# Optimization experiments

Measured on AMD Instinct MI355X. Metric: run time of the kernel, lower is better.

The kernel has to match this reference:

```python
import jax, jax.numpy as jnp
import numpy as np

B, N, NR, D = 1024, 100000, 500, 200
OC, FW = 32, 9          # out_channels, filt_w (filt_h is always 1)
L = D - FW + 1          # 192, conv output width
EPS = 1e-5


def setup_inputs() -> dict:
    key = jax.random.key(0)
    ks = jax.random.split(key, 22)
    inp = {
        "e1_idx": jax.random.randint(ks[0], (B,), 0, N),
        "r_idx": jax.random.randint(ks[1], (B,), 0, NR),
        "E": jax.random.normal(ks[2], (N, D), jnp.float32) * 0.1,
        "R": jax.random.normal(ks[3], (NR, D), jnp.float32) * 0.1,
        "W_fc": jax.random.normal(ks[4], (OC * L, D), jnp.float32) * 0.02,
        "b_fc": jnp.zeros((D,), jnp.float32),
        "W_fc1": jax.random.normal(ks[5], (D, OC * FW), jnp.float32) * 0.05,
        "b_fc1": jnp.zeros((OC * FW,), jnp.float32),
        "bn0_g": jax.random.uniform(ks[6], (1,), jnp.float32, 0.5, 1.5),
        "bn0_b": jax.random.normal(ks[7], (1,), jnp.float32) * 0.1,
        "bn0_m": jax.random.normal(ks[8], (1,), jnp.float32) * 0.1,
        "bn0_v": jax.random.uniform(ks[9], (1,), jnp.float32, 0.5, 1.5),
        "bn1_g": jax.random.uniform(ks[10], (OC,), jnp.float32, 0.5, 1.5),
        "bn1_b": jax.random.normal(ks[11], (OC,), jnp.float32) * 0.1,
        "bn1_m": jax.random.normal(ks[12], (OC,), jnp.float32) * 0.1,
        "bn1_v": jax.random.uniform(ks[13], (OC,), jnp.float32, 0.5, 1.5),
        "bn2_g": jax.random.uniform(ks[14], (D,), jnp.float32, 0.5, 1.5),
        "bn2_b": jax.random.normal(ks[15], (D,), jnp.float32) * 0.1,
        "bn2_m": jax.random.normal(ks[16], (D,), jnp.float32) * 0.1,
        "bn2_v": jax.random.uniform(ks[17], (D,), jnp.float32, 0.5, 1.5),
        "b": jnp.zeros((N,), jnp.float32),
    }
    return inp


def reference(e1_idx, r_idx, E, R, W_fc, b_fc, W_fc1, b_fc1,
              bn0_g, bn0_b, bn0_m, bn0_v,
              bn1_g, bn1_b, bn1_m, bn1_v,
              bn2_g, bn2_b, bn2_m, bn2_v, b):
    # embeddings
    e1 = E[e1_idx]                       # [B, D]  (the [B,1,1,D] image)
    r = R[r_idx]                         # [B, D]
    # bn0 over the single input channel (eval mode, running stats)
    x = (e1 - bn0_m) * (bn0_g / jnp.sqrt(bn0_v + EPS)) + bn0_b   # [B, D]
    # hypernetwork: per-sample filters
    k = (r @ W_fc1 + b_fc1).reshape(B, OC, FW)                    # [B, OC, FW]
    # per-sample grouped conv == sliding-window batched small matmul
    idx = jnp.arange(L)[:, None] + jnp.arange(FW)[None, :]        # [L, FW]
    win = x[:, idx]                                               # [B, L, FW]
    y = jnp.einsum('blw,bow->bol', win, k)                        # [B, OC, L]
    # bn1 over OC channels (eval)
    y = (y - bn1_m[:, None]) * (bn1_g / jnp.sqrt(bn1_v + EPS))[:, None] + bn1_b[:, None]
    # fc (torch Linear: x @ W.T + b, W_fc is [fc_len, D])
    h = y.reshape(B, OC * L) @ W_fc + b_fc                        # [B, D]
    # bn2 over D features (eval) + relu
    h = (h - bn2_m) * (bn2_g / jnp.sqrt(bn2_v + EPS)) + bn2_b
    h = jax.nn.relu(h)
    # score against all entities
    logits = h @ E.T + b                                          # [B, N]
    return jax.nn.sigmoid(logits)
```

## Files before the change

kernel.cpp:

```cpp
#include <hip/hip_runtime.h>

#define B_    1024
#define N_    100000
#define NP_   100096
#define NR_   500
#define D_    200
#define KP_   224
#define OC_   32
#define FW_   9
#define L_    192
#define OCL_  6144
#define KS_   16
#define KCH_  384
#define EPS_  1e-5f

typedef __attribute__((ext_vector_type(8))) short  bf16x8;
typedef __attribute__((ext_vector_type(4))) float  f32x4;

static __device__ __forceinline__ unsigned short f2bf(float x) {
    unsigned int u = __float_as_uint(x);
    unsigned int r = (u + 0x7FFFu + ((u >> 16) & 1u)) >> 16;
    return (unsigned short)r;
}

__global__ __launch_bounds__(256) void k1(
    const int* __restrict__ e1_idx, const int* __restrict__ r_idx,
    const float* __restrict__ E, const float* __restrict__ R,
    const float* __restrict__ W_fc1, const float* __restrict__ b_fc1,
    const float* __restrict__ W_fc,
    const float* __restrict__ bn0_g, const float* __restrict__ bn0_b,
    const float* __restrict__ bn0_m, const float* __restrict__ bn0_v,
    const float* __restrict__ bn1_g, const float* __restrict__ bn1_b,
    const float* __restrict__ bn1_m, const float* __restrict__ bn1_v,
    unsigned short* __restrict__ y_bf, unsigned short* __restrict__ Wt_bf,
    unsigned short* __restrict__ E_bf)
{
    const int tid = threadIdx.x;
    const int bid = blockIdx.x;

    if (bid < B_) {
        __shared__ float x_lds[D_];
        __shared__ float r_lds[D_];
        __shared__ float k_lds[OC_ * FW_];
        __shared__ float s1_lds[OC_], t1_lds[OC_];

        const int b = bid;
        const float s0 = bn0_g[0] / sqrtf(bn0_v[0] + EPS_);
        const float c0 = bn0_b[0] - bn0_m[0] * s0;

        if (tid < D_) {
            x_lds[tid] = E[(long)e1_idx[b] * D_ + tid] * s0 + c0;
            r_lds[tid] = R[(long)r_idx[b] * D_ + tid];
        } else if (tid >= 224) {
            int o = tid - 224;
            float s1 = bn1_g[o] / sqrtf(bn1_v[o] + EPS_);
            s1_lds[o] = s1;
            t1_lds[o] = bn1_b[o] - bn1_m[o] * s1;
        }
        __syncthreads();

        for (int j = tid; j < OC_ * FW_; j += 256) {
            float acc = b_fc1[j];
            #pragma unroll 4
            for (int d = 0; d < D_; ++d)
                acc += r_lds[d] * W_fc1[d * (OC_ * FW_) + j];
            k_lds[j] = acc * s1_lds[j / FW_];
        }
        __syncthreads();

        unsigned short* yrow = y_bf + (long)b * OCL_;
        for (int idx = tid; idx < OCL_; idx += 256) {
            int o = idx / L_;
            int l = idx - o * L_;
            const float* kp = &k_lds[o * FW_];
            float acc = t1_lds[o];
            #pragma unroll
            for (int w = 0; w < FW_; ++w)
                acc += x_lds[l + w] * kp[w];
            yrow[idx] = f2bf(acc);
        }
    } else if (bid < B_ + 384) {
        __shared__ float t_lds[64][65];
        const int wb = bid - B_;
        const int k0 = (wb % 96) * 64;
        const int d0 = (wb / 96) * 64;
        const int c  = tid & 63;
        const int r4 = tid >> 6;
        #pragma unroll
        for (int i = 0; i < 16; ++i) {
            int row = i * 4 + r4;
            t_lds[row][c] = (d0 + c < D_) ? W_fc[(long)(k0 + row) * D_ + d0 + c] : 0.f;
        }
        __syncthreads();
        #pragma unroll
        for (int i = 0; i < 16; ++i) {
            int drow = i * 4 + r4;
            Wt_bf[(long)(d0 + drow) * OCL_ + k0 + c] = f2bf(t_lds[c][drow]);
        }
    } else {
        long id = (long)(bid - (B_ + 384)) * 256 + tid;
        int n = (int)(id / (KP_ / 4));
        int cc = (int)(id - (long)n * (KP_ / 4));
        ushort4 o = {0, 0, 0, 0};
        if (n < N_ && cc < D_ / 4) {
            float4 v = *(const float4*)&E[(long)n * D_ + cc * 4];
            o.x = f2bf(v.x); o.y = f2bf(v.y); o.z = f2bf(v.z); o.w = f2bf(v.w);
        }
        *(ushort4*)&E_bf[(long)n * KP_ + cc * 4] = o;
    }
}

__global__ __launch_bounds__(256) void kB(
    const unsigned short* __restrict__ y_bf, const unsigned short* __restrict__ Wt_bf,
    float* __restrict__ pre)
{
    const int wave = threadIdx.x >> 6;
    const int lane = threadIdx.x & 63;
    const int quad = lane >> 4;
    const int lc   = lane & 15;

    const int m0 = blockIdx.x * 128 + wave * 32;
    const int n0 = blockIdx.y * 64;
    const int kb = blockIdx.z * KCH_;

    f32x4 acc[2][4] = {};

    const short* a0p = (const short*)y_bf + (long)(m0 + lc) * OCL_ + kb + quad * 8;
    const short* a1p = a0p + 16 * OCL_;

    #pragma unroll
    for (int k0 = 0; k0 < KCH_; k0 += 32) {
        bf16x8 a0 = *(const bf16x8*)(a0p + k0);
        bf16x8 a1 = *(const bf16x8*)(a1p + k0);
        #pragma unroll
        for (int t = 0; t < 4; ++t) {
            bf16x8 bv = *(const bf16x8*)((const short*)Wt_bf
                         + (long)(n0 + t * 16 + lc) * OCL_ + kb + k0 + quad * 8);
            acc[0][t] = __builtin_amdgcn_mfma_f32_16x16x32_bf16(a0, bv, acc[0][t], 0, 0, 0);
            acc[1][t] = __builtin_amdgcn_mfma_f32_16x16x32_bf16(a1, bv, acc[1][t], 0, 0, 0);
        }
    }

    #pragma unroll
    for (int t = 0; t < 4; ++t) {
        int d = n0 + t * 16 + lc;
        if (d < KP_) {
            #pragma unroll
            for (int mi = 0; mi < 2; ++mi)
                #pragma unroll
                for (int r = 0; r < 4; ++r) {
                    int m = m0 + mi * 16 + quad * 4 + r;
                    pre[((long)blockIdx.z * B_ + m) * KP_ + d] = acc[mi][t][r];
                }
        }
    }
}

__global__ __launch_bounds__(256) void kB2(
    const float* __restrict__ pre, const float* __restrict__ b_fc,
    const float* __restrict__ bn2_g, const float* __restrict__ bn2_b,
    const float* __restrict__ bn2_m, const float* __restrict__ bn2_v,
    unsigned short* __restrict__ h_bf)
{
    int id = blockIdx.x * 256 + threadIdx.x;
    if (id >= B_ * KP_) return;
    int b = id / KP_;
    int d = id - b * KP_;
    float h = 0.f;
    if (d < D_) {
        float s = 0.f;
        #pragma unroll
        for (int sp = 0; sp < KS_; ++sp)
            s += pre[(long)sp * B_ * KP_ + id];
        float s2 = bn2_g[d] / sqrtf(bn2_v[d] + EPS_);
        h = (s + b_fc[d] - bn2_m[d]) * s2 + bn2_b[d];
        h = fmaxf(h, 0.f);
    }
    h_bf[id] = f2bf(h);
}

__global__ __launch_bounds__(256) void kE(
    const float* __restrict__ E, unsigned short* __restrict__ E_bf)
{
    long id = (long)blockIdx.x * 256 + threadIdx.x;
    if (id >= (long)NP_ * (KP_ / 4)) return;
    int n = (int)(id / (KP_ / 4));
    int c = (int)(id - (long)n * (KP_ / 4));
    ushort4 o = {0, 0, 0, 0};
    if (n < N_ && c < D_ / 4) {
        float4 v = *(const float4*)&E[(long)n * D_ + c * 4];
        o.x = f2bf(v.x); o.y = f2bf(v.y); o.z = f2bf(v.z); o.w = f2bf(v.w);
    }
    *(ushort4*)&E_bf[(long)n * KP_ + c * 4] = o;
}

__global__ __launch_bounds__(256) void kC(
    const unsigned short* __restrict__ h_bf, const unsigned short* __restrict__ E_bf,
    const float* __restrict__ bias, float* __restrict__ out)
{
    __shared__ short smem[64 * 256];

    const int tid  = threadIdx.x;
    const int wave = tid >> 6;
    const int lane = tid & 63;
    const int quad = lane >> 4;
    const int lc   = lane & 15;

    const int m0 = blockIdx.x * 128 + wave * 32;
    const int n0 = blockIdx.y * 64;

    {
        const short* src = (const short*)E_bf;
        #pragma unroll
        for (int i = 0; i < 7; ++i) {
            int u   = tid + i * 256;
            int row = u / 28;
            int c16 = u - row * 28;
            int4 v = *(const int4*)(src + (long)(n0 + row) * KP_ + c16 * 8);
            int c = c16 ^ (row & 7);
            *(int4*)&smem[row * 256 + c * 8] = v;
        }
    }
    __syncthreads();

    f32x4 acc[2][4] = {};

    const short* hbase0 = (const short*)h_bf + (long)(m0 + lc) * KP_ + quad * 8;
    const short* hbase1 = hbase0 + 16 * KP_;

    #pragma unroll
    for (int k0 = 0; k0 < KP_; k0 += 32) {
        bf16x8 a0 = *(const bf16x8*)(hbase0 + k0);
        bf16x8 a1 = *(const bf16x8*)(hbase1 + k0);
        const int cbase = (k0 >> 3) + quad;
        #pragma unroll
        for (int t = 0; t < 4; ++t) {
            int row = t * 16 + lc;
            int c   = cbase ^ (row & 7);
            bf16x8 bv = *(const bf16x8*)&smem[row * 256 + c * 8];
            acc[0][t] = __builtin_amdgcn_mfma_f32_16x16x32_bf16(a0, bv, acc[0][t], 0, 0, 0);
            acc[1][t] = __builtin_amdgcn_mfma_f32_16x16x32_bf16(a1, bv, acc[1][t], 0, 0, 0);
        }
    }

    __syncthreads();
    float* fw = (float*)smem + wave * 2048;

    #pragma unroll
    for (int t = 0; t < 4; ++t) {
        int n = n0 + t * 16 + lc;
        float bv = (n < N_) ? bias[n] : 0.f;
        #pragma unroll
        for (int mi = 0; mi < 2; ++mi)
            #pragma unroll
            for (int r = 0; r < 4; ++r) {
                int rl = mi * 16 + quad * 4 + r;
                fw[rl * 64 + t * 16 + lc] = acc[mi][t][r] + bv;
            }
    }

    #pragma unroll
    for (int j = 0; j < 8; ++j) {
        int u  = lane + j * 64;
        int rl = u >> 4;
        int c4 = u & 15;
        int n  = n0 + c4 * 4;
        if (n < N_) {
            float4 v = *(const float4*)&fw[rl * 64 + c4 * 4];
            float4 o;
            o.x = 1.f / (1.f + __expf(-v.x));
            o.y = 1.f / (1.f + __expf(-v.y));
            o.z = 1.f / (1.f + __expf(-v.z));
            o.w = 1.f / (1.f + __expf(-v.w));
            *(float4*)&out[(long)(m0 + rl) * N_ + n] = o;
        }
    }
}

extern "C" void kernel_launch(void* const* d_in, const int* in_sizes, int n_in,
                              void* d_out, int out_size, void* d_ws, size_t ws_size,
                              hipStream_t stream) {
    const int*   e1_idx = (const int*)d_in[0];
    const int*   r_idx  = (const int*)d_in[1];
    const float* E      = (const float*)d_in[2];
    const float* R      = (const float*)d_in[3];
    const float* W_fc   = (const float*)d_in[4];
    const float* b_fc   = (const float*)d_in[5];
    const float* W_fc1  = (const float*)d_in[6];
    const float* b_fc1  = (const float*)d_in[7];
    const float* bn0_g  = (const float*)d_in[8];
    const float* bn0_b  = (const float*)d_in[9];
    const float* bn0_m  = (const float*)d_in[10];
    const float* bn0_v  = (const float*)d_in[11];
    const float* bn1_g  = (const float*)d_in[12];
    const float* bn1_b  = (const float*)d_in[13];
    const float* bn1_m  = (const float*)d_in[14];
    const float* bn1_v  = (const float*)d_in[15];
    const float* bn2_g  = (const float*)d_in[16];
    const float* bn2_b  = (const float*)d_in[17];
    const float* bn2_m  = (const float*)d_in[18];
    const float* bn2_v  = (const float*)d_in[19];
    const float* bias   = (const float*)d_in[20];
    float* out = (float*)d_out;

    char* base = (char*)d_ws;
    unsigned short* y_bf  = (unsigned short*)(base);
    float*          pre   = (float*)(base + 12582912L);
    unsigned short* Wt_bf = (unsigned short*)(base + 27262976L);
    unsigned short* h_bf  = (unsigned short*)(base + 44843008L);
    const size_t FLAT_NEED = 90144768UL;
    const bool flat = ws_size >= FLAT_NEED;
    unsigned short* E_bf = flat ? (unsigned short*)(base + 45301760L)
                                : (unsigned short*)(base);

    const int ECONV_BLOCKS = (int)(((long)NP_ * (KP_ / 4)) / 256);
    const int k1_blocks = flat ? (B_ + 384 + ECONV_BLOCKS) : (B_ + 384);

    k1<<<k1_blocks, 256, 0, stream>>>(e1_idx, r_idx, E, R, W_fc1, b_fc1, W_fc,
                                      bn0_g, bn0_b, bn0_m, bn0_v,
                                      bn1_g, bn1_b, bn1_m, bn1_v,
                                      y_bf, Wt_bf, E_bf);
    kB<<<dim3(8, 4, KS_), 256, 0, stream>>>(y_bf, Wt_bf, pre);
    kB2<<<(B_ * KP_ + 255) / 256, 256, 0, stream>>>(pre, b_fc, bn2_g, bn2_b, bn2_m, bn2_v, h_bf);
    if (!flat)
        kE<<<ECONV_BLOCKS, 256, 0, stream>>>(E, E_bf);
    kC<<<dim3(8, NP_ / 64), 256, 0, stream>>>(h_bf, E_bf, bias, out);
}
```

Baseline: 673.7 us.

## Fuse E bf16 conversion into scoring GEMM load and remap block order

Removes the separate pass that converted the whole entity table to a padded bf16 buffer. The scoring kernel now reads fp32 rows of E directly, converts them to bf16 while filling LDS, and zero-pads columns and out-of-range rows itself. Blocks are also launched on a 1D grid remapped so that consecutive blocks are spread across the 8 batch tiles. The intent is to stop writing and rereading a ~45MB intermediate. In exchange each E tile is read as fp32 and converted by all 8 batch-tile blocks that share it, rather than once.

```diff
diff --git a/kernel.cpp b/kernel.cpp
--- a/kernel.cpp
+++ b/kernel.cpp
@@ -12,6 +12,7 @@
 #define OCL_  6144
 #define KS_   16
 #define KCH_  384
+#define NT_   1564
 #define EPS_  1e-5f
 
 typedef __attribute__((ext_vector_type(8))) short  bf16x8;
@@ -32,8 +33,7 @@
     const float* __restrict__ bn0_m, const float* __restrict__ bn0_v,
     const float* __restrict__ bn1_g, const float* __restrict__ bn1_b,
     const float* __restrict__ bn1_m, const float* __restrict__ bn1_v,
-    unsigned short* __restrict__ y_bf, unsigned short* __restrict__ Wt_bf,
-    unsigned short* __restrict__ E_bf)
+    unsigned short* __restrict__ y_bf, unsigned short* __restrict__ Wt_bf)
 {
     const int tid = threadIdx.x;
     const int bid = blockIdx.x;
@@ -79,7 +79,7 @@
                 acc += x_lds[l + w] * kp[w];
             yrow[idx] = f2bf(acc);
         }
-    } else if (bid < B_ + 384) {
+    } else {
         __shared__ float t_lds[64][65];
         const int wb = bid - B_;
         const int k0 = (wb % 96) * 64;
@@ -97,16 +97,6 @@
             int drow = i * 4 + r4;
             Wt_bf[(long)(d0 + drow) * OCL_ + k0 + c] = f2bf(t_lds[c][drow]);
         }
-    } else {
-        long id = (long)(bid - (B_ + 384)) * 256 + tid;
-        int n = (int)(id / (KP_ / 4));
-        int cc = (int)(id - (long)n * (KP_ / 4));
-        ushort4 o = {0, 0, 0, 0};
-        if (n < N_ && cc < D_ / 4) {
-            float4 v = *(const float4*)&E[(long)n * D_ + cc * 4];
-            o.x = f2bf(v.x); o.y = f2bf(v.y); o.z = f2bf(v.z); o.w = f2bf(v.w);
-        }
-        *(ushort4*)&E_bf[(long)n * KP_ + cc * 4] = o;
     }
 }
 
@@ -179,23 +169,8 @@
     h_bf[id] = f2bf(h);
 }
 
-__global__ __launch_bounds__(256) void kE(
-    const float* __restrict__ E, unsigned short* __restrict__ E_bf)
-{
-    long id = (long)blockIdx.x * 256 + threadIdx.x;
-    if (id >= (long)NP_ * (KP_ / 4)) return;
-    int n = (int)(id / (KP_ / 4));
-    int c = (int)(id - (long)n * (KP_ / 4));
-    ushort4 o = {0, 0, 0, 0};
-    if (n < N_ && c < D_ / 4) {
-        float4 v = *(const float4*)&E[(long)n * D_ + c * 4];
-        o.x = f2bf(v.x); o.y = f2bf(v.y); o.z = f2bf(v.z); o.w = f2bf(v.w);
-    }
-    *(ushort4*)&E_bf[(long)n * KP_ + c * 4] = o;
-}
-
 __global__ __launch_bounds__(256) void kC(
-    const unsigned short* __restrict__ h_bf, const unsigned short* __restrict__ E_bf,
+    const unsigned short* __restrict__ h_bf, const float* __restrict__ E,
     const float* __restrict__ bias, float* __restrict__ out)
 {
     __shared__ short smem[64 * 256];
@@ -206,19 +181,25 @@
     const int quad = lane >> 4;
     const int lc   = lane & 15;
 
-    const int m0 = blockIdx.x * 128 + wave * 32;
-    const int n0 = blockIdx.y * 64;
+    const int bid = blockIdx.x;
+    const int g   = (bid & 7) * NT_ + (bid >> 3);
+    const int m0  = (g & 7) * 128 + wave * 32;
+    const int n0  = (g >> 3) * 64;
 
     {
-        const short* src = (const short*)E_bf;
-        #pragma unroll
-        for (int i = 0; i < 7; ++i) {
+        #pragma unroll
+        for (int i = 0; i < 14; ++i) {
             int u   = tid + i * 256;
-            int row = u / 28;
-            int c16 = u - row * 28;
-            int4 v = *(const int4*)(src + (long)(n0 + row) * KP_ + c16 * 8);
-            int c = c16 ^ (row & 7);
-            *(int4*)&smem[row * 256 + c * 8] = v;
+            int row = u / 56;
+            int s8  = u - row * 56;
+            int n   = n0 + row;
+            ushort4 o = {0, 0, 0, 0};
+            if (n < N_ && s8 < 50) {
+                float4 v = *(const float4*)&E[(long)n * D_ + s8 * 4];
+                o.x = f2bf(v.x); o.y = f2bf(v.y); o.z = f2bf(v.z); o.w = f2bf(v.w);
+            }
+            int c16 = s8 >> 1, half = s8 & 1;
+            *(ushort4*)&smem[row * 256 + ((c16 ^ (row & 7)) << 3) + half * 4] = o;
         }
     }
     __syncthreads();
@@ -308,21 +289,12 @@
     float*          pre   = (float*)(base + 12582912L);
     unsigned short* Wt_bf = (unsigned short*)(base + 27262976L);
     unsigned short* h_bf  = (unsigned short*)(base + 44843008L);
-    const size_t FLAT_NEED = 90144768UL;
-    const bool flat = ws_size >= FLAT_NEED;
-    unsigned short* E_bf = flat ? (unsigned short*)(base + 45301760L)
-                                : (unsigned short*)(base);
-
-    const int ECONV_BLOCKS = (int)(((long)NP_ * (KP_ / 4)) / 256);
-    const int k1_blocks = flat ? (B_ + 384 + ECONV_BLOCKS) : (B_ + 384);
-
-    k1<<<k1_blocks, 256, 0, stream>>>(e1_idx, r_idx, E, R, W_fc1, b_fc1, W_fc,
-                                      bn0_g, bn0_b, bn0_m, bn0_v,
-                                      bn1_g, bn1_b, bn1_m, bn1_v,
-                                      y_bf, Wt_bf, E_bf);
+
+    k1<<<B_ + 384, 256, 0, stream>>>(e1_idx, r_idx, E, R, W_fc1, b_fc1, W_fc,
+                                     bn0_g, bn0_b, bn0_m, bn0_v,
+                                     bn1_g, bn1_b, bn1_m, bn1_v,
+                                     y_bf, Wt_bf);
     kB<<<dim3(8, 4, KS_), 256, 0, stream>>>(y_bf, Wt_bf, pre);
     kB2<<<(B_ * KP_ + 255) / 256, 256, 0, stream>>>(pre, b_fc, bn2_g, bn2_b, bn2_m, bn2_v, h_bf);
-    if (!flat)
-        kE<<<ECONV_BLOCKS, 256, 0, stream>>>(E, E_bf);
-    kC<<<dim3(8, NP_ / 64), 256, 0, stream>>>(h_bf, E_bf, bias, out);
-}
+    kC<<<8 * NT_, 256, 0, stream>>>(h_bf, E, bias, out);
+}
```

Result: slower. 733.3 us (+8.8%).
